# Performance work log

Hardware: AMD Instinct MI355X
Metric: run time of the kernel (lower is better)

## Reference

```python
import jax, jax.numpy as jnp
import numpy as np

D_MODEL = 1024
H = 16
D_K = D_MODEL // H
NEG_INF = -1e9


def setup_inputs() -> dict:
    key = jax.random.key(0)
    ks = jax.random.split(key, 12)
    B, S = 2, 2048
    s = 1.0 / np.sqrt(D_MODEL)
    inp = {
        "query": jax.random.normal(ks[0], (B, S, D_MODEL), jnp.float32),
        "key": jax.random.normal(ks[1], (B, S, D_MODEL), jnp.float32),
        "value": jax.random.normal(ks[2], (B, S, D_MODEL), jnp.float32),
        "mask": jnp.ones((B, 1, 1, S), jnp.int32),
        "w_q": jax.random.normal(ks[3], (D_MODEL, D_MODEL), jnp.float32) * s,
        "b_q": jax.random.normal(ks[4], (D_MODEL,), jnp.float32) * s,
        "w_k": jax.random.normal(ks[5], (D_MODEL, D_MODEL), jnp.float32) * s,
        "b_k": jax.random.normal(ks[6], (D_MODEL,), jnp.float32) * s,
        "w_v": jax.random.normal(ks[7], (D_MODEL, D_MODEL), jnp.float32) * s,
        "b_v": jax.random.normal(ks[8], (D_MODEL,), jnp.float32) * s,
        "w_o": jax.random.normal(ks[9], (D_MODEL, D_MODEL), jnp.float32) * s,
        "b_o": jax.random.normal(ks[10], (D_MODEL,), jnp.float32) * s,
    }
    return inp


def _split_heads(x):
    B, S, _ = x.shape
    return x.reshape(B, S, H, D_K).transpose(0, 2, 1, 3)  # (B,H,S,d_k)


def reference(query, key, value, mask, w_q, b_q, w_k, b_k, w_v, b_v, w_o, b_o):
    # torch Linear: y = x @ W^T + b
    q = _split_heads(query @ w_q.T + b_q)
    k = _split_heads(key @ w_k.T + b_k)
    v = _split_heads(value @ w_v.T + b_v)
    scale = 1.0 / jnp.sqrt(jnp.asarray(D_K, q.dtype))
    scores = jnp.einsum("bhqd,bhkd->bhqk", q, k) * scale  # (B,H,Sq,Sk)
    scores = jnp.where(mask == 0, jnp.asarray(NEG_INF, scores.dtype), scores)
    attn = jax.nn.softmax(scores, axis=-1)
    ctx = jnp.einsum("bhqk,bhkd->bhqd", attn, v)
    B, _, Sq, _ = ctx.shape
    ctx = ctx.transpose(0, 2, 1, 3).reshape(B, Sq, D_MODEL)
    out = ctx @ w_o.T + b_o
    return out, attn
```

## Files before the change

kernel.cpp:

```cpp
#include <hip/hip_runtime.h>
#include <math.h>

#define MDIM 4096
#define NDIM 1024
#define KDIM 1024
#define S_LEN 2048
#define NH 16
#define DK 64
#define KT 64
#define QT 64
#define NTILE (S_LEN / KT)

__global__ __launch_bounds__(256, 4)
void gemm_nt_kernel(const float* __restrict__ A, const float* __restrict__ W,
                    const float* __restrict__ bias, float* __restrict__ Y,
                    int split_head)
{
    __shared__ float As[64][68];
    __shared__ float Ws[64][68];
    const int tid = threadIdx.x;
    const int m0 = blockIdx.y << 6;
    const int n0 = blockIdx.x << 6;
    const int tx = tid & 15;
    const int ty = tid >> 4;
    const int srow = tid >> 2;
    const int sc4  = tid & 3;

    const float4* asrc = (const float4*)(A + (size_t)(m0 + srow) * KDIM) + sc4;
    const float4* wsrc = (const float4*)(W + (size_t)(n0 + srow) * KDIM) + sc4;

    float4 ar[4], wr[4];
    #pragma unroll
    for (int i = 0; i < 4; i++) { ar[i] = asrc[i << 2]; wr[i] = wsrc[i << 2]; }

    float acc[4][4] = {};

    for (int k0 = 0; k0 < KDIM; k0 += 64) {
        __syncthreads();
        #pragma unroll
        for (int i = 0; i < 4; i++) {
            int d = (sc4 + (i << 2)) << 2;
            As[d + 0][srow] = ar[i].x; As[d + 1][srow] = ar[i].y;
            As[d + 2][srow] = ar[i].z; As[d + 3][srow] = ar[i].w;
            Ws[d + 0][srow] = wr[i].x; Ws[d + 1][srow] = wr[i].y;
            Ws[d + 2][srow] = wr[i].z; Ws[d + 3][srow] = wr[i].w;
        }
        __syncthreads();
        if (k0 + 64 < KDIM) {
            asrc += 16; wsrc += 16;
            #pragma unroll
            for (int i = 0; i < 4; i++) { ar[i] = asrc[i << 2]; wr[i] = wsrc[i << 2]; }
        }
        #pragma unroll 8
        for (int kk = 0; kk < 64; kk++) {
            float a[4], w[4];
            *(float4*)a = *(const float4*)&As[kk][ty << 2];
            *(float4*)w = *(const float4*)&Ws[kk][tx << 2];
            #pragma unroll
            for (int i = 0; i < 4; i++)
                #pragma unroll
                for (int j = 0; j < 4; j++)
                    acc[i][j] += a[i] * w[j];
        }
    }

    #pragma unroll
    for (int i = 0; i < 4; i++) {
        int m = m0 + (ty << 2) + i;
        #pragma unroll
        for (int j = 0; j < 4; j++) {
            int n = n0 + (tx << 2) + j;
            float val = acc[i][j] + bias[n];
            if (split_head) {
                int b = m >> 11, s = m & (S_LEN - 1);
                int h = n >> 6,  d = n & (DK - 1);
                Y[(((size_t)(b * NH + h) * S_LEN + s) << 6) + d] = val;
            } else {
                Y[(size_t)m * NDIM + n] = val;
            }
        }
    }
}

__global__ __launch_bounds__(256, 4)
void attn_kernel(const float* __restrict__ q, const float* __restrict__ k,
                 const float* __restrict__ v, const int* __restrict__ mask,
                 float* __restrict__ attn, float* __restrict__ ctx)
{
    const int b   = blockIdx.z;
    const int h   = blockIdx.y;
    const int q0  = blockIdx.x << 6;
    const int tid = threadIdx.x;
    const int tx  = tid & 15;
    const int ty  = tid >> 4;

    __shared__ float Qs[64][68];
    __shared__ float Ks[64][68];
    float (*Vs)[68] = Qs;
    float* Ps = &Ks[0][0];

    const float* qbase = q + (((size_t)(b * NH + h) * S_LEN + q0) << 6);
    const float* kbase = k + (((size_t)(b * NH + h) * S_LEN) << 6);
    const float* vbase = v + (((size_t)(b * NH + h) * S_LEN) << 6);
    const int*   mrow  = mask + b * S_LEN;

    const int srow = tid >> 2;
    const int sc4  = tid & 3;

    {
        const float4* src = (const float4*)(qbase + ((size_t)srow << 6)) + sc4;
        #pragma unroll
        for (int i = 0; i < 4; i++) {
            float4 t = src[i << 2];
            int d = (sc4 + (i << 2)) << 2;
            Qs[d + 0][srow] = t.x; Qs[d + 1][srow] = t.y;
            Qs[d + 2][srow] = t.z; Qs[d + 3][srow] = t.w;
        }
    }

    const float scale = 0.125f;
    float mr[4], lr[4];
    #pragma unroll
    for (int i = 0; i < 4; i++) { mr[i] = -1e30f; lr[i] = 0.f; }

    const size_t abase = ((size_t)((b * NH + h) * S_LEN + q0 + (ty << 2))) * S_LEN
                       + (tx << 2);

    const float4* ksrc = (const float4*)(kbase + ((size_t)srow << 6)) + sc4;
    float4 kr[4];
    #pragma unroll
    for (int i = 0; i < 4; i++) kr[i] = ksrc[i << 2];

    for (int t = 0; t < NTILE; t++) {
        __syncthreads();
        #pragma unroll
        for (int i = 0; i < 4; i++) {
            int d = (sc4 + (i << 2)) << 2;
            Ks[d + 0][srow] = kr[i].x; Ks[d + 1][srow] = kr[i].y;
            Ks[d + 2][srow] = kr[i].z; Ks[d + 3][srow] = kr[i].w;
        }
        __syncthreads();
        if (t + 1 < NTILE) {
            ksrc += 1024;
            #pragma unroll
            for (int i = 0; i < 4; i++) kr[i] = ksrc[i << 2];
        }

        float s[4][4] = {};
        #pragma unroll 8
        for (int kk = 0; kk < 64; kk++) {
            float a[4], w[4];
            *(float4*)a = *(const float4*)&Qs[kk][ty << 2];
            *(float4*)w = *(const float4*)&Ks[kk][tx << 2];
            #pragma unroll
            for (int i = 0; i < 4; i++)
                #pragma unroll
                for (int j = 0; j < 4; j++)
                    s[i][j] += a[i] * w[j];
        }

        int4 mk = ((const int4*)(mrow + (t << 6)))[tx];
        #pragma unroll
        for (int i = 0; i < 4; i++) {
            s[i][0] = (mk.x == 0) ? -1e9f : s[i][0] * scale;
            s[i][1] = (mk.y == 0) ? -1e9f : s[i][1] * scale;
            s[i][2] = (mk.z == 0) ? -1e9f : s[i][2] * scale;
            s[i][3] = (mk.w == 0) ? -1e9f : s[i][3] * scale;
            float mt = fmaxf(fmaxf(s[i][0], s[i][1]), fmaxf(s[i][2], s[i][3]));
            float mn = fmaxf(mr[i], mt);
            lr[i] = lr[i] * __expf(mr[i] - mn)
                  + __expf(s[i][0] - mn) + __expf(s[i][1] - mn)
                  + __expf(s[i][2] - mn) + __expf(s[i][3] - mn);
            mr[i] = mn;
            *(float4*)(attn + abase + (t << 6) + (size_t)i * S_LEN) =
                make_float4(s[i][0], s[i][1], s[i][2], s[i][3]);
        }
    }

    #pragma unroll
    for (int off = 1; off < 16; off <<= 1) {
        #pragma unroll
        for (int i = 0; i < 4; i++) {
            float m2 = __shfl_xor(mr[i], off);
            float l2 = __shfl_xor(lr[i], off);
            float mn = fmaxf(mr[i], m2);
            lr[i] = lr[i] * __expf(mr[i] - mn) + l2 * __expf(m2 - mn);
            mr[i] = mn;
        }
    }
    float invl[4];
    #pragma unroll
    for (int i = 0; i < 4; i++) invl[i] = 1.0f / lr[i];

    const int vrow = tid >> 4;
    const int vc4  = tid & 15;

    float acc[4][4] = {};
    float4 vr[4], sr[4];
    #pragma unroll
    for (int i = 0; i < 4; i++) {
        vr[i] = ((const float4*)(vbase + (((size_t)(vrow + (i << 4))) << 6)))[vc4];
        sr[i] = *(const float4*)(attn + abase + (size_t)i * S_LEN);
    }

    for (int t = 0; t < NTILE; t++) {
        __syncthreads();
        #pragma unroll
        for (int i = 0; i < 4; i++)
            *(float4*)&Vs[vrow + (i << 4)][vc4 << 2] = vr[i];

        float p[4][4];
        #pragma unroll
        for (int i = 0; i < 4; i++) {
            p[i][0] = __expf(sr[i].x - mr[i]) * invl[i];
            p[i][1] = __expf(sr[i].y - mr[i]) * invl[i];
            p[i][2] = __expf(sr[i].z - mr[i]) * invl[i];
            p[i][3] = __expf(sr[i].w - mr[i]) * invl[i];
            *(float4*)(attn + abase + (t << 6) + (size_t)i * S_LEN) =
                make_float4(p[i][0], p[i][1], p[i][2], p[i][3]);
        }
        #pragma unroll
        for (int j = 0; j < 4; j++)
            *(float4*)&Ps[(size_t)((tx << 2) + j) * 68 + (ty << 2)] =
                make_float4(p[0][j], p[1][j], p[2][j], p[3][j]);
        __syncthreads();

        if (t + 1 < NTILE) {
            #pragma unroll
            for (int i = 0; i < 4; i++) {
                vr[i] = ((const float4*)(vbase +
                          ((((size_t)(t + 1) << 6) + vrow + (i << 4)) << 6)))[vc4];
                sr[i] = *(const float4*)(attn + abase + ((t + 1) << 6)
                                         + (size_t)i * S_LEN);
            }
        }

        #pragma unroll 8
        for (int kk = 0; kk < 64; kk++) {
            float pa[4], wv[4];
            *(float4*)pa = *(const float4*)&Ps[(size_t)kk * 68 + (ty << 2)];
            *(float4*)wv = *(const float4*)&Vs[kk][tx << 2];
            #pragma unroll
            for (int i = 0; i < 4; i++)
                #pragma unroll
                for (int j = 0; j < 4; j++)
                    acc[i][j] += pa[i] * wv[j];
        }
    }

    #pragma unroll
    for (int i = 0; i < 4; i++) {
        int row = q0 + (ty << 2) + i;
        *(float4*)(ctx + (((size_t)(b * S_LEN + row) * NH + h) << 6) + (tx << 2)) =
            make_float4(acc[i][0], acc[i][1], acc[i][2], acc[i][3]);
    }
}

extern "C" void kernel_launch(void* const* d_in, const int* in_sizes, int n_in,
                              void* d_out, int out_size, void* d_ws, size_t ws_size,
                              hipStream_t stream)
{
    const float* query = (const float*)d_in[0];
    const float* key   = (const float*)d_in[1];
    const float* value = (const float*)d_in[2];
    const int*   mask  = (const int*)d_in[3];
    const float* w_q = (const float*)d_in[4];
    const float* b_q = (const float*)d_in[5];
    const float* w_k = (const float*)d_in[6];
    const float* b_k = (const float*)d_in[7];
    const float* w_v = (const float*)d_in[8];
    const float* b_v = (const float*)d_in[9];
    const float* w_o = (const float*)d_in[10];
    const float* b_o = (const float*)d_in[11];

    float* out  = (float*)d_out;
    float* attn = (float*)d_out + (size_t)4194304;

    float* qws  = (float*)d_ws;
    float* kws  = qws + 4194304;
    float* vws  = kws + 4194304;
    float* ctxw = vws + 4194304;

    dim3 gemm_grid(NDIM / 64, MDIM / 64);
    dim3 block(256);

    hipLaunchKernelGGL(gemm_nt_kernel, gemm_grid, block, 0, stream, query, w_q, b_q, qws, 1);
    hipLaunchKernelGGL(gemm_nt_kernel, gemm_grid, block, 0, stream, key,   w_k, b_k, kws, 1);
    hipLaunchKernelGGL(gemm_nt_kernel, gemm_grid, block, 0, stream, value, w_v, b_v, vws, 1);

    dim3 attn_grid(S_LEN / QT, NH, 2);
    hipLaunchKernelGGL(attn_kernel, attn_grid, block, 0, stream, qws, kws, vws, mask, attn, ctxw);

    hipLaunchKernelGGL(gemm_nt_kernel, gemm_grid, block, 0, stream, ctxw, w_o, b_o, out, 0);
}
```

Before: 1.651 ms.

## Enlarge projection GEMM tile to 128x64 and vectorize epilogue stores

Each GEMM block now computes a 128x64 output tile, with every thread accumulating an 8x4 register tile, so each loaded W element is reused across twice as many rows. Launch bounds drop to 2 blocks per SM and the grid halves along M. The epilogue loads bias as a float4 and writes float4 rows in both the split-head and plain layouts. The aim is fewer LDS/global loads per FMA, at the cost of higher register and shared memory use and fewer blocks in flight.

```diff
diff --git a/kernel.cpp b/kernel.cpp
--- a/kernel.cpp
+++ b/kernel.cpp
@@ -11,72 +11,87 @@
 #define QT 64
 #define NTILE (S_LEN / KT)
 
-__global__ __launch_bounds__(256, 4)
+__global__ __launch_bounds__(256, 2)
 void gemm_nt_kernel(const float* __restrict__ A, const float* __restrict__ W,
                     const float* __restrict__ bias, float* __restrict__ Y,
                     int split_head)
 {
-    __shared__ float As[64][68];
+    __shared__ float As[64][132];
     __shared__ float Ws[64][68];
     const int tid = threadIdx.x;
-    const int m0 = blockIdx.y << 6;
+    const int m0 = blockIdx.y << 7;
     const int n0 = blockIdx.x << 6;
     const int tx = tid & 15;
     const int ty = tid >> 4;
-    const int srow = tid >> 2;
-    const int sc4  = tid & 3;
-
-    const float4* asrc = (const float4*)(A + (size_t)(m0 + srow) * KDIM) + sc4;
-    const float4* wsrc = (const float4*)(W + (size_t)(n0 + srow) * KDIM) + sc4;
-
-    float4 ar[4], wr[4];
-    #pragma unroll
-    for (int i = 0; i < 4; i++) { ar[i] = asrc[i << 2]; wr[i] = wsrc[i << 2]; }
-
-    float acc[4][4] = {};
-
-    for (int k0 = 0; k0 < KDIM; k0 += 64) {
-        __syncthreads();
-        #pragma unroll
-        for (int i = 0; i < 4; i++) {
-            int d = (sc4 + (i << 2)) << 2;
-            As[d + 0][srow] = ar[i].x; As[d + 1][srow] = ar[i].y;
-            As[d + 2][srow] = ar[i].z; As[d + 3][srow] = ar[i].w;
-            Ws[d + 0][srow] = wr[i].x; Ws[d + 1][srow] = wr[i].y;
-            Ws[d + 2][srow] = wr[i].z; Ws[d + 3][srow] = wr[i].w;
-        }
-        __syncthreads();
-        if (k0 + 64 < KDIM) {
+
+    const int arow = tid >> 1;
+    const int ac4  = tid & 1;
+    const int wrow = tid >> 2;
+    const int wc4  = tid & 3;
+
+    const float4* asrc = (const float4*)(A + (size_t)(m0 + arow) * KDIM) + ac4;
+    const float4* wsrc = (const float4*)(W + (size_t)(n0 + wrow) * KDIM) + wc4;
+
+    float4 ar[8], wr[4];
+    #pragma unroll
+    for (int i = 0; i < 8; i++) ar[i] = asrc[i << 1];
+    #pragma unroll
+    for (int i = 0; i < 4; i++) wr[i] = wsrc[i << 2];
+
+    float acc[2][4][4] = {};
+
+    for (int t = 0; t < 16; t++) {
+        __syncthreads();
+        #pragma unroll
+        for (int i = 0; i < 8; i++) {
+            int c = (ac4 + (i << 1)) << 2;
+            As[c + 0][arow] = ar[i].x; As[c + 1][arow] = ar[i].y;
+            As[c + 2][arow] = ar[i].z; As[c + 3][arow] = ar[i].w;
+        }
+        #pragma unroll
+        for (int i = 0; i < 4; i++) {
+            int c = (wc4 + (i << 2)) << 2;
+            Ws[c + 0][wrow] = wr[i].x; Ws[c + 1][wrow] = wr[i].y;
+            Ws[c + 2][wrow] = wr[i].z; Ws[c + 3][wrow] = wr[i].w;
+        }
+        __syncthreads();
+        if (t + 1 < 16) {
             asrc += 16; wsrc += 16;
             #pragma unroll
-            for (int i = 0; i < 4; i++) { ar[i] = asrc[i << 2]; wr[i] = wsrc[i << 2]; }
+            for (int i = 0; i < 8; i++) ar[i] = asrc[i << 1];
+            #pragma unroll
+            for (int i = 0; i < 4; i++) wr[i] = wsrc[i << 2];
         }
         #pragma unroll 8
         for (int kk = 0; kk < 64; kk++) {
-            float a[4], w[4];
-            *(float4*)a = *(const float4*)&As[kk][ty << 2];
-            *(float4*)w = *(const float4*)&Ws[kk][tx << 2];
+            float a0[4], a1[4], w[4];
+            *(float4*)a0 = *(const float4*)&As[kk][ty << 2];
+            *(float4*)a1 = *(const float4*)&As[kk][64 + (ty << 2)];
+            *(float4*)w  = *(const float4*)&Ws[kk][tx << 2];
             #pragma unroll
             for (int i = 0; i < 4; i++)
                 #pragma unroll
-                for (int j = 0; j < 4; j++)
-                    acc[i][j] += a[i] * w[j];
-        }
-    }
-
-    #pragma unroll
-    for (int i = 0; i < 4; i++) {
-        int m = m0 + (ty << 2) + i;
-        #pragma unroll
-        for (int j = 0; j < 4; j++) {
-            int n = n0 + (tx << 2) + j;
-            float val = acc[i][j] + bias[n];
+                for (int j = 0; j < 4; j++) {
+                    acc[0][i][j] += a0[i] * w[j];
+                    acc[1][i][j] += a1[i] * w[j];
+                }
+        }
+    }
+
+    float4 b4 = ((const float4*)(bias + n0))[tx];
+    #pragma unroll
+    for (int p = 0; p < 2; p++) {
+        #pragma unroll
+        for (int i = 0; i < 4; i++) {
+            int m = m0 + (p << 6) + (ty << 2) + i;
+            float4 val = make_float4(acc[p][i][0] + b4.x, acc[p][i][1] + b4.y,
+                                     acc[p][i][2] + b4.z, acc[p][i][3] + b4.w);
             if (split_head) {
                 int b = m >> 11, s = m & (S_LEN - 1);
-                int h = n >> 6,  d = n & (DK - 1);
-                Y[(((size_t)(b * NH + h) * S_LEN + s) << 6) + d] = val;
+                int h = n0 >> 6;
+                *(float4*)(Y + (((size_t)(b * NH + h) * S_LEN + s) << 6) + (tx << 2)) = val;
             } else {
-                Y[(size_t)m * NDIM + n] = val;
+                *(float4*)(Y + (size_t)m * NDIM + n0 + (tx << 2)) = val;
             }
         }
     }
@@ -281,7 +296,7 @@
     float* vws  = kws + 4194304;
     float* ctxw = vws + 4194304;
 
-    dim3 gemm_grid(NDIM / 64, MDIM / 64);
+    dim3 gemm_grid(NDIM / 64, MDIM / 128);
     dim3 block(256);
 
     hipLaunchKernelGGL(gemm_nt_kernel, gemm_grid, block, 0, stream, query, w_q, b_q, qws, 1);
```

Measured after the change: 1.651 ms. About the same (+0.0%).
